# Performance work log

Hardware: AMD Instinct MI355X
Metric: run time of the kernel (lower is better)

## Reference

```python
import jax, jax.numpy as jnp
import numpy as np

N_NODES = 100000


def sage_layer(h, src, dst, w_self, w_neigh, b):
    """DGL SAGEConv with mean aggregator: fc_self(h) + fc_neigh(mean_in_neigh(h)) + b."""
    msg = h[src]  # [E, d] gather source features
    agg = jax.ops.segment_sum(msg, dst, num_segments=N_NODES)  # [N, d]
    deg = jax.ops.segment_sum(jnp.ones((src.shape[0],), h.dtype), dst, num_segments=N_NODES)
    mean = agg / jnp.maximum(deg, 1.0)[:, None]
    return h @ w_self + mean @ w_neigh + b


def setup_inputs() -> dict:
    key = jax.random.key(0)
    ks = jax.random.split(key, 12)
    N, E = N_NODES, 1600000
    in_f, hid, n_cls = 4, 128, 2

    def glorot(k, shape):
        lim = float(np.sqrt(6.0 / (shape[0] + shape[1])))
        return jax.random.uniform(k, shape, jnp.float32, -lim, lim)

    return {
        "feats": jax.random.normal(ks[0], (N, in_f), jnp.float32),
        "src": jax.random.randint(ks[1], (E,), 0, N),
        "dst": jax.random.randint(ks[2], (E,), 0, N),
        "w_self1": glorot(ks[3], (in_f, hid)),
        "w_neigh1": glorot(ks[4], (in_f, hid)),
        "b1": jnp.zeros((hid,), jnp.float32),
        "w_self2": glorot(ks[5], (hid, hid)),
        "w_neigh2": glorot(ks[6], (hid, hid)),
        "b2": jnp.zeros((hid,), jnp.float32),
        "w_out": glorot(ks[7], (hid, n_cls)),
        "b_out": jnp.zeros((n_cls,), jnp.float32),
    }


def reference(feats, src, dst, w_self1, w_neigh1, b1, w_self2, w_neigh2, b2, w_out, b_out):
    h = jax.nn.relu(sage_layer(feats, src, dst, w_self1, w_neigh1, b1))
    h = jax.nn.relu(sage_layer(h, src, dst, w_self2, w_neigh2, b2))
    return h @ w_out + b_out  # [N, num_classes] logits
```

## Files before the change

kernel.cpp:

```cpp
#include <hip/hip_runtime.h>
#include <hip/hip_bf16.h>

static constexpr int N = 100000;
static constexpr int HID = 128;
static constexpr int NBKT = (N + 127) / 128;
static constexpr int BCAP = 2560;
static constexpr int BEPB = 4096;

typedef short v8s __attribute__((ext_vector_type(8)));
typedef float v4f __attribute__((ext_vector_type(4)));
typedef unsigned short u16x8 __attribute__((ext_vector_type(8)));

static __device__ __forceinline__ unsigned short f2bf(float x) {
  unsigned u = __float_as_uint(x);
  return (unsigned short)((u + 0x7fffu + ((u >> 16) & 1u)) >> 16);
}
static __device__ __forceinline__ float bf2f(unsigned short u) {
  return __uint_as_float(((unsigned)u) << 16);
}

__global__ void k_wprep(const float* __restrict__ ws2, const float* __restrict__ wn2,
                        unsigned short* __restrict__ wp, unsigned* __restrict__ bcur) {
  int id = blockIdx.x * 64 + threadIdx.x;
  if (id < NBKT) bcur[id] = (unsigned)id * BCAP;
  int b = blockIdx.x;
  int mat = b >> 5;
  int ks = (b >> 3) & 3;
  int cf = b & 7;
  int l = threadIdx.x;
  const float* W = mat ? wn2 : ws2;
  int col = cf * 16 + (l & 15);
  int k0 = ks * 32 + (l >> 4) * 8;
  u16x8 h8, l8;
#pragma unroll
  for (int i = 0; i < 8; ++i) {
    float w = W[(k0 + i) * 128 + col];
    unsigned short h = f2bf(w);
    h8[i] = h;
    l8[i] = f2bf(w - bf2f(h));
  }
  int fhi = (ks * 4 + mat) * 8 + cf;
  int flo = (ks * 4 + mat + 2) * 8 + cf;
  *reinterpret_cast<u16x8*>(wp + fhi * 512 + l * 8) = h8;
  *reinterpret_cast<u16x8*>(wp + flo * 512 + l * 8) = l8;
}

__global__ __launch_bounds__(256) void k_bucket(const int* __restrict__ src,
                                                const int* __restrict__ dst,
                                                unsigned* __restrict__ bcur,
                                                unsigned* __restrict__ bucket, int E) {
  __shared__ unsigned hist[NBKT];
  __shared__ unsigned base[NBKT];
  for (int i = threadIdx.x; i < NBKT; i += 256) hist[i] = 0;
  __syncthreads();
  const int e0 = blockIdx.x * BEPB;
  const int n = min(e0 + BEPB, E) - e0;

  unsigned pk[16];
  int bk[16];
#pragma unroll
  for (int i = 0; i < 16; ++i) {
    int e = threadIdx.x + 256 * i;
    if (e < n) {
      int d = __builtin_nontemporal_load(dst + e0 + e);
      int s = __builtin_nontemporal_load(src + e0 + e);
      int b = d >> 7;
      pk[i] = ((unsigned)s << 7) | (unsigned)(d & 127);
      bk[i] = b;
      atomicAdd(&hist[b], 1u);
    } else {
      bk[i] = -1;
      pk[i] = 0;
    }
  }
  __syncthreads();
  for (int i = threadIdx.x; i < NBKT; i += 256) {
    unsigned h = hist[i];
    base[i] = h ? atomicAdd(&bcur[i], h) : 0u;
    hist[i] = 0;
  }
  __syncthreads();
#pragma unroll
  for (int i = 0; i < 16; ++i) {
    if (bk[i] >= 0) {
      unsigned pos = base[bk[i]] + atomicAdd(&hist[bk[i]], 1u);
      bucket[pos] = pk[i];
    }
  }
}

__global__ void k_bucketscan(const unsigned* __restrict__ bcur, unsigned* __restrict__ bbase) {
  __shared__ unsigned s[1024];
  int t = threadIdx.x;
  unsigned v = (t < NBKT) ? (bcur[t] - (unsigned)t * BCAP) : 0u;
  s[t] = v;
  __syncthreads();
  for (int off = 1; off < 1024; off <<= 1) {
    unsigned x = (t >= off) ? s[t - off] : 0u;
    __syncthreads();
    s[t] += x;
    __syncthreads();
  }
  if (t < NBKT) bbase[t] = s[t] - v;
}

__global__ __launch_bounds__(256) void k_csr(const unsigned* __restrict__ bcur,
                                             const unsigned* __restrict__ bbase,
                                             const unsigned* __restrict__ bucket,
                                             unsigned* __restrict__ cnt,
                                             unsigned* __restrict__ roff,
                                             int* __restrict__ csr) {
  const int b = blockIdx.x;
  const unsigned segbase = (unsigned)b * BCAP;
  const unsigned n = bcur[b] - segbase;
  const int v0 = b << 7;
  __shared__ unsigned h[128];
  __shared__ unsigned rowoff[128];
  __shared__ unsigned s[128];
  if (threadIdx.x < 128) h[threadIdx.x] = 0;
  __syncthreads();

  unsigned pk[10];
#pragma unroll
  for (int i = 0; i < 10; ++i) {
    unsigned idx = threadIdx.x + 256u * i;
    if (idx < n) {
      pk[i] = bucket[segbase + idx];
      atomicAdd(&h[pk[i] & 127u], 1u);
    } else {
      pk[i] = 0xffffffffu;
    }
  }
  __syncthreads();

  unsigned val = (threadIdx.x < 128) ? h[threadIdx.x] : 0u;
  if (threadIdx.x < 128) s[threadIdx.x] = val;
  __syncthreads();
  for (int off = 1; off < 128; off <<= 1) {
    unsigned x = (threadIdx.x < 128 && threadIdx.x >= off) ? s[threadIdx.x - off] : 0u;
    __syncthreads();
    if (threadIdx.x < 128) s[threadIdx.x] += x;
    __syncthreads();
  }
  if (threadIdx.x < 128) {
    int v = v0 + threadIdx.x;
    if (v < N) {
      unsigned rstart = bbase[b] + s[threadIdx.x] - val;
      rowoff[threadIdx.x] = rstart;
      roff[v] = rstart;
      cnt[v] = val;
    }
    h[threadIdx.x] = 0;
  }
  __syncthreads();

#pragma unroll
  for (int i = 0; i < 10; ++i) {
    if (pk[i] != 0xffffffffu) {
      unsigned dl = pk[i] & 127u;
      unsigned pos = rowoff[dl] + atomicAdd(&h[dl], 1u);
      csr[pos] = (int)(pk[i] >> 7);
    }
  }
}

__global__ void k_layer1(const float* __restrict__ feats, const unsigned* __restrict__ cnt,
                         const unsigned* __restrict__ roff, const int* __restrict__ csr,
                         const float* __restrict__ ws1, const float* __restrict__ wn1,
                         const float* __restrict__ b1, unsigned short* __restrict__ h1) {
  const int v = blockIdx.x * 16 + (threadIdx.x >> 4);
  const int l = threadIdx.x & 15;
  if (v >= N) return;
  const unsigned c = cnt[v];
  const unsigned start = roff[v];
  float4 acc = make_float4(0.f, 0.f, 0.f, 0.f);
  for (unsigned e = l; e < c; e += 16) {
    int s = csr[start + e];
    float4 f = *reinterpret_cast<const float4*>(feats + 4 * s);
    acc.x += f.x; acc.y += f.y; acc.z += f.z; acc.w += f.w;
  }
#pragma unroll
  for (int off = 1; off < 16; off <<= 1) {
    acc.x += __shfl_xor(acc.x, off);
    acc.y += __shfl_xor(acc.y, off);
    acc.z += __shfl_xor(acc.z, off);
    acc.w += __shfl_xor(acc.w, off);
  }
  float inv = 1.0f / fmaxf((float)c, 1.0f);
  float m0 = acc.x * inv, m1 = acc.y * inv, m2 = acc.z * inv, m3 = acc.w * inv;
  float4 fv = *reinterpret_cast<const float4*>(feats + 4 * v);
  const int c0 = l * 8;
  unsigned o[4];
#pragma unroll
  for (int half = 0; half < 2; ++half) {
    float4 bv = *reinterpret_cast<const float4*>(b1 + c0 + 4 * half);
    float ob[4] = {bv.x, bv.y, bv.z, bv.w};
#pragma unroll
    for (int k = 0; k < 4; ++k) {
      float4 wsv = *reinterpret_cast<const float4*>(ws1 + k * 128 + c0 + 4 * half);
      float4 wnv = *reinterpret_cast<const float4*>(wn1 + k * 128 + c0 + 4 * half);
      float fk = (k == 0) ? fv.x : (k == 1) ? fv.y : (k == 2) ? fv.z : fv.w;
      float mk = (k == 0) ? m0 : (k == 1) ? m1 : (k == 2) ? m2 : m3;
      ob[0] += fk * wsv.x + mk * wnv.x;
      ob[1] += fk * wsv.y + mk * wnv.y;
      ob[2] += fk * wsv.z + mk * wnv.z;
      ob[3] += fk * wsv.w + mk * wnv.w;
    }
#pragma unroll
    for (int jj = 0; jj < 2; ++jj) {
      float lo = fmaxf(ob[2 * jj], 0.f), hi = fmaxf(ob[2 * jj + 1], 0.f);
      o[2 * half + jj] = (unsigned)f2bf(lo) | (((unsigned)f2bf(hi)) << 16);
    }
  }
  *reinterpret_cast<uint4*>(h1 + (size_t)v * HID + c0) =
      make_uint4(o[0], o[1], o[2], o[3]);
}

__global__ __launch_bounds__(256) void k_agg_l2(
    const unsigned* __restrict__ cnt, const unsigned* __restrict__ roff,
    const int* __restrict__ csr, const unsigned short* __restrict__ h1,
    const unsigned short* __restrict__ wp, const float* __restrict__ b2,
    const float* __restrict__ wout, const float* __restrict__ bout,
    float* __restrict__ out) {
  __shared__ unsigned short mlds[64][136];
  const int t = threadIdx.x;
  const int wv = t >> 6;
  const int lane = t & 63;
  const int hl = lane & 31;
  const int half = lane >> 5;
  const int vbase = blockIdx.x * 64;

  const unsigned short* __restrict__ hrow = h1 + hl * 4;
#pragma unroll 1
  for (int p = 0; p < 8; ++p) {
    const int vl = wv * 16 + 2 * p + half;
    const int v = vbase + vl;
    unsigned c = 0, start = 0;
    if (v < N) { c = cnt[v]; start = roff[v]; }
    float x0 = 0.f, x1 = 0.f, x2 = 0.f, x3 = 0.f;
    float y0 = 0.f, y1 = 0.f, y2 = 0.f, y3 = 0.f;
    const unsigned cm = c & ~3u;
    unsigned e = 0;
    for (; e < cm; e += 4) {
      int s[4];
#pragma unroll
      for (int q = 0; q < 4; ++q) s[q] = csr[start + e + q];
      uint2 pk[4];
#pragma unroll
      for (int q = 0; q < 4; ++q)
        pk[q] = *reinterpret_cast<const uint2*>(hrow + (size_t)s[q] * HID);
#pragma unroll
      for (int q = 0; q < 4; ++q) {
        float f0 = __uint_as_float(pk[q].x << 16);
        float f1 = __uint_as_float(pk[q].x & 0xffff0000u);
        float f2 = __uint_as_float(pk[q].y << 16);
        float f3 = __uint_as_float(pk[q].y & 0xffff0000u);
        if (q & 1) { y0 += f0; y1 += f1; y2 += f2; y3 += f3; }
        else       { x0 += f0; x1 += f1; x2 += f2; x3 += f3; }
      }
    }
    for (; e < c; ++e) {
      int s = csr[start + e];
      uint2 pk = *reinterpret_cast<const uint2*>(hrow + (size_t)s * HID);
      x0 += __uint_as_float(pk.x << 16);
      x1 += __uint_as_float(pk.x & 0xffff0000u);
      x2 += __uint_as_float(pk.y << 16);
      x3 += __uint_as_float(pk.y & 0xffff0000u);
    }
    float inv = 1.0f / fmaxf((float)c, 1.0f);
    x0 = (x0 + y0) * inv; x1 = (x1 + y1) * inv;
    x2 = (x2 + y2) * inv; x3 = (x3 + y3) * inv;
    uint2 o;
    o.x = (unsigned)f2bf(x0) | (((unsigned)f2bf(x1)) << 16);
    o.y = (unsigned)f2bf(x2) | (((unsigned)f2bf(x3)) << 16);
    *reinterpret_cast<uint2*>(&mlds[vl][hl * 4]) = o;
  }
  __syncthreads();

  const int rlane = lane & 15;
  const int kg = lane >> 4;
  v4f acc[8];
#pragma unroll
  for (int cf = 0; cf < 8; ++cf) acc[cf] = (v4f)(0.f);

  size_t hr = (size_t)vbase + wv * 16 + rlane;
  if (hr >= N) hr = N - 1;
#pragma unroll
  for (int ks = 0; ks < 4; ++ks) {
    v8s ah = *reinterpret_cast<const v8s*>(h1 + hr * HID + ks * 32 + kg * 8);
    v8s am = *reinterpret_cast<const v8s*>(&mlds[wv * 16 + rlane][ks * 32 + kg * 8]);
#pragma unroll
    for (int m = 0; m < 4; ++m) {
#pragma unroll
      for (int cf = 0; cf < 8; ++cf) {
        v8s bf = *reinterpret_cast<const v8s*>(wp + ((ks * 4 + m) * 8 + cf) * 512 + lane * 8);
        acc[cf] = __builtin_amdgcn_mfma_f32_16x16x32_bf16(
            (m & 1) ? am : ah, bf, acc[cf], 0, 0, 0);
      }
    }
  }

  float b2c[8], w0c[8], w1c[8];
#pragma unroll
  for (int cf = 0; cf < 8; ++cf) {
    int col = cf * 16 + rlane;
    b2c[cf] = b2[col];
    w0c[cf] = wout[col * 2 + 0];
    w1c[cf] = wout[col * 2 + 1];
  }
  const float bo0 = bout[0], bo1 = bout[1];
#pragma unroll
  for (int j = 0; j < 4; ++j) {
    float s0 = 0.f, s1 = 0.f;
#pragma unroll
    for (int cf = 0; cf < 8; ++cf) {
      float h2 = fmaxf(acc[cf][j] + b2c[cf], 0.f);
      s0 += h2 * w0c[cf];
      s1 += h2 * w1c[cf];
    }
#pragma unroll
    for (int off = 1; off < 16; off <<= 1) {
      s0 += __shfl_xor(s0, off);
      s1 += __shfl_xor(s1, off);
    }
    size_t row = (size_t)vbase + wv * 16 + kg * 4 + j;
    if (row < N) {
      if (rlane == 0) out[row * 2 + 0] = s0 + bo0;
      if (rlane == 1) out[row * 2 + 1] = s1 + bo1;
    }
  }
}

extern "C" void kernel_launch(void* const* d_in, const int* in_sizes, int n_in,
                              void* d_out, int out_size, void* d_ws, size_t ws_size,
                              hipStream_t stream) {
  const float* feats = (const float*)d_in[0];
  const int* src = (const int*)d_in[1];
  const int* dst = (const int*)d_in[2];
  const float* ws1 = (const float*)d_in[3];
  const float* wn1 = (const float*)d_in[4];
  const float* b1 = (const float*)d_in[5];
  const float* ws2 = (const float*)d_in[6];
  const float* wn2 = (const float*)d_in[7];
  const float* b2 = (const float*)d_in[8];
  const float* wout = (const float*)d_in[9];
  const float* bout = (const float*)d_in[10];
  float* out = (float*)d_out;
  const int E = in_sizes[1];

  char* p = (char*)d_ws;
  unsigned* bcur = (unsigned*)p;             p += 784 * 4;
  unsigned* bbase = (unsigned*)p;            p += 784 * 4;
  unsigned* bucket = (unsigned*)p;           p += (size_t)NBKT * BCAP * 4;
  int* csr = (int*)p;                        p += (size_t)E * 4;
  unsigned* cnt = (unsigned*)p;              p += (size_t)N * 4;
  unsigned* roff = (unsigned*)p;             p += (size_t)N * 4;
  unsigned short* h1 = (unsigned short*)p;   p += (size_t)N * HID * 2;
  unsigned short* wp = (unsigned short*)p;

  int bgrid = (E + BEPB - 1) / BEPB;
  k_wprep<<<64, 64, 0, stream>>>(ws2, wn2, wp, bcur);
  k_bucket<<<bgrid, 256, 0, stream>>>(src, dst, bcur, bucket, E);
  k_bucketscan<<<1, 1024, 0, stream>>>(bcur, bbase);
  k_csr<<<NBKT, 256, 0, stream>>>(bcur, bbase, bucket, cnt, roff, csr);
  k_layer1<<<(N + 15) / 16, 256, 0, stream>>>(feats, cnt, roff, csr, ws1, wn1, b1, h1);
  k_agg_l2<<<(N + 63) / 64, 256, 0, stream>>>(cnt, roff, csr, h1, wp, b2, wout, bout, out);
}
```

Baseline: 191.0 us.

## Split layer-2 GEMM across waves by output column and shrink blocks to sixteen nodes

The layer-2 aggregation plus GEMM kernel now processes 16 nodes per 512-thread block instead of 64 nodes per 256-thread block. Each wave aggregates two nodes once, then computes one 16-column slice of the 128-wide output with MFMA. Per-wave partial logits are reduced through shared memory. This raises the number of blocks and the parallelism per node, and cuts per-wave register pressure from eight accumulators to one. The cost is an extra barrier and shared-memory reduction, and the removed bounds checks rely on N being divisible by 16.

```diff
diff --git a/kernel.cpp b/kernel.cpp
--- a/kernel.cpp
+++ b/kernel.cpp
@@ -216,27 +216,27 @@
       make_uint4(o[0], o[1], o[2], o[3]);
 }
 
-__global__ __launch_bounds__(256) void k_agg_l2(
+__global__ __launch_bounds__(512) void k_agg_l2(
     const unsigned* __restrict__ cnt, const unsigned* __restrict__ roff,
     const int* __restrict__ csr, const unsigned short* __restrict__ h1,
     const unsigned short* __restrict__ wp, const float* __restrict__ b2,
     const float* __restrict__ wout, const float* __restrict__ bout,
     float* __restrict__ out) {
-  __shared__ unsigned short mlds[64][136];
+  __shared__ unsigned short mlds[16][132];
+  __shared__ float2 plds[8][16];
   const int t = threadIdx.x;
   const int wv = t >> 6;
   const int lane = t & 63;
   const int hl = lane & 31;
   const int half = lane >> 5;
-  const int vbase = blockIdx.x * 64;
-
-  const unsigned short* __restrict__ hrow = h1 + hl * 4;
-#pragma unroll 1
-  for (int p = 0; p < 8; ++p) {
-    const int vl = wv * 16 + 2 * p + half;
+  const int vbase = blockIdx.x * 16;
+
+  {
+    const int vl = wv * 2 + half;
     const int v = vbase + vl;
-    unsigned c = 0, start = 0;
-    if (v < N) { c = cnt[v]; start = roff[v]; }
+    const unsigned c = cnt[v];
+    const unsigned start = roff[v];
+    const unsigned short* __restrict__ hrow = h1 + hl * 4;
     float x0 = 0.f, x1 = 0.f, x2 = 0.f, x3 = 0.f;
     float y0 = 0.f, y1 = 0.f, y2 = 0.f, y3 = 0.f;
     const unsigned cm = c & ~3u;
@@ -279,55 +279,45 @@
 
   const int rlane = lane & 15;
   const int kg = lane >> 4;
-  v4f acc[8];
-#pragma unroll
-  for (int cf = 0; cf < 8; ++cf) acc[cf] = (v4f)(0.f);
-
-  size_t hr = (size_t)vbase + wv * 16 + rlane;
-  if (hr >= N) hr = N - 1;
+  const int cf = wv;
+  v4f acc = (v4f)(0.f);
 #pragma unroll
   for (int ks = 0; ks < 4; ++ks) {
-    v8s ah = *reinterpret_cast<const v8s*>(h1 + hr * HID + ks * 32 + kg * 8);
-    v8s am = *reinterpret_cast<const v8s*>(&mlds[wv * 16 + rlane][ks * 32 + kg * 8]);
+    v8s ah = *reinterpret_cast<const v8s*>(h1 + (size_t)(vbase + rlane) * HID + ks * 32 + kg * 8);
+    v8s am = *reinterpret_cast<const v8s*>(&mlds[rlane][ks * 32 + kg * 8]);
 #pragma unroll
     for (int m = 0; m < 4; ++m) {
-#pragma unroll
-      for (int cf = 0; cf < 8; ++cf) {
-        v8s bf = *reinterpret_cast<const v8s*>(wp + ((ks * 4 + m) * 8 + cf) * 512 + lane * 8);
-        acc[cf] = __builtin_amdgcn_mfma_f32_16x16x32_bf16(
-            (m & 1) ? am : ah, bf, acc[cf], 0, 0, 0);
-      }
-    }
-  }
-
-  float b2c[8], w0c[8], w1c[8];
-#pragma unroll
-  for (int cf = 0; cf < 8; ++cf) {
-    int col = cf * 16 + rlane;
-    b2c[cf] = b2[col];
-    w0c[cf] = wout[col * 2 + 0];
-    w1c[cf] = wout[col * 2 + 1];
-  }
-  const float bo0 = bout[0], bo1 = bout[1];
+      v8s bf = *reinterpret_cast<const v8s*>(wp + ((ks * 4 + m) * 8 + cf) * 512 + lane * 8);
+      acc = __builtin_amdgcn_mfma_f32_16x16x32_bf16((m & 1) ? am : ah, bf, acc, 0, 0, 0);
+    }
+  }
+
+  const float b2c = b2[cf * 16 + rlane];
+  const float w0c = wout[(cf * 16 + rlane) * 2 + 0];
+  const float w1c = wout[(cf * 16 + rlane) * 2 + 1];
 #pragma unroll
   for (int j = 0; j < 4; ++j) {
-    float s0 = 0.f, s1 = 0.f;
-#pragma unroll
-    for (int cf = 0; cf < 8; ++cf) {
-      float h2 = fmaxf(acc[cf][j] + b2c[cf], 0.f);
-      s0 += h2 * w0c[cf];
-      s1 += h2 * w1c[cf];
-    }
+    float h2 = fmaxf(acc[j] + b2c, 0.f);
+    float s0 = h2 * w0c;
+    float s1 = h2 * w1c;
 #pragma unroll
     for (int off = 1; off < 16; off <<= 1) {
       s0 += __shfl_xor(s0, off);
       s1 += __shfl_xor(s1, off);
     }
-    size_t row = (size_t)vbase + wv * 16 + kg * 4 + j;
-    if (row < N) {
-      if (rlane == 0) out[row * 2 + 0] = s0 + bo0;
-      if (rlane == 1) out[row * 2 + 1] = s1 + bo1;
-    }
+    if (rlane == 0) plds[wv][kg * 4 + j] = make_float2(s0, s1);
+  }
+  __syncthreads();
+
+  if (t < 16) {
+    float s0 = bout[0], s1 = bout[1];
+#pragma unroll
+    for (int w = 0; w < 8; ++w) {
+      float2 pv = plds[w][t];
+      s0 += pv.x;
+      s1 += pv.y;
+    }
+    *reinterpret_cast<float2*>(out + (size_t)(vbase + t) * 2) = make_float2(s0, s1);
   }
 }
 
@@ -364,5 +354,5 @@
   k_bucketscan<<<1, 1024, 0, stream>>>(bcur, bbase);
   k_csr<<<NBKT, 256, 0, stream>>>(bcur, bbase, bucket, cnt, roff, csr);
   k_layer1<<<(N + 15) / 16, 256, 0, stream>>>(feats, cnt, roff, csr, ws1, wn1, b1, h1);
-  k_agg_l2<<<(N + 63) / 64, 256, 0, stream>>>(cnt, roff, csr, h1, wp, b2, wout, bout, out);
-}
+  k_agg_l2<<<N / 16, 512, 0, stream>>>(cnt, roff, csr, h1, wp, b2, wout, bout, out);
+}
```

Measured after the change: 176.2 us. -7.7%, faster.
